# Kernel tuning notes

Measured on AMD Instinct MI355X. Metric: run time of the kernel, lower is better.

The kernel has to match this reference:

```python
import jax, jax.numpy as jnp
import numpy as np

B, DZ, M_, N_ = 2048, 256, 64, 64
GAMMA, EPS, MAXITERS = 1.0, 1e-6, 1000


def sinkhorn(Mcost):
    # entropic OT with uniform marginals r=1/m, c=1/n (ddn sinkhorn, non-logspace)
    b, h, w = Mcost.shape
    r = 1.0 / h
    c = 1.0 / w
    P = jnp.exp(-GAMMA * Mcost)
    P = P / jnp.sum(P, axis=(1, 2), keepdims=True)

    def cond_fn(state):
        P, it, err = state
        return jnp.logical_and(it < MAXITERS, err > EPS)

    def body_fn(state):
        P, it, _ = state
        alpha = jnp.sum(P, axis=2, keepdims=True)   # row sums (B,h,1)
        P = P * (r / alpha)                          # row normalize to r
        beta = jnp.sum(P, axis=1, keepdims=True)    # col sums (B,1,w)
        err = jnp.max(jnp.abs(beta - c))
        # torch loop breaks BEFORE col-normalizing when converged
        P = jnp.where(err <= EPS, P, P * (c / beta))
        return P, it + 1, err

    init_err = jnp.array(jnp.inf, dtype=Mcost.dtype)
    P, _, _ = jax.lax.while_loop(cond_fn, body_fn, (P, jnp.array(0, jnp.int32), init_err))
    return P


def setup_inputs() -> dict:
    key = jax.random.key(0)
    ks = jax.random.split(key, 7)
    H = M_ * N_
    z = jax.random.normal(ks[0], (B, DZ), dtype=jnp.float32)
    W1 = jax.random.normal(ks[1], (DZ, H), dtype=jnp.float32) * (1.0 / np.sqrt(DZ))
    b1 = jnp.zeros((H,), jnp.float32)
    W2 = jax.random.normal(ks[2], (H, H), dtype=jnp.float32) * (1.0 / np.sqrt(H))
    b2 = jnp.zeros((H,), jnp.float32)
    W3 = jax.random.normal(ks[3], (H, H), dtype=jnp.float32) * (1.0 / np.sqrt(H))
    b3 = jnp.zeros((H,), jnp.float32)
    return {"z": z, "W1": W1, "b1": b1, "W2": W2, "b2": b2, "W3": W3, "b3": b3}


def reference(z, W1, b1, W2, b2, W3, b3):
    x = jax.nn.relu(z @ W1 + b1)
    x = jax.nn.relu(x @ W2 + b2)
    x = x @ W3 + b3
    x = x.reshape(z.shape[0], M_, N_)  # (B, m, n) cost matrix
    return sinkhorn(x)
```

## Files before the change

### kernel.cpp

```cpp
#include <hip/hip_runtime.h>
#include <hip/hip_bf16.h>

typedef unsigned short ushort_t;
typedef __attribute__((ext_vector_type(8))) short bf16x8;
typedef __attribute__((ext_vector_type(4))) float f32x4;

#define MDIM 2048
#define NDIM 4096

__device__ __forceinline__ ushort_t to_bf16(float f) {
    __hip_bfloat16 h = __float2bfloat16(f);
    return *reinterpret_cast<ushort_t*>(&h);
}

__global__ void cast_bf16_kernel(const float* __restrict__ in, ushort_t* __restrict__ out, int n) {
    int i = blockIdx.x * blockDim.x + threadIdx.x;
    if (i < n) out[i] = to_bf16(in[i]);
}

__global__ void transpose_cast_kernel(const float* __restrict__ W, ushort_t* __restrict__ WT,
                                      int K, int N) {
    __shared__ float tile[32][33];
    const int tx = threadIdx.x, ty = threadIdx.y;
    const int n0 = blockIdx.x * 32, k0 = blockIdx.y * 32;
#pragma unroll
    for (int r = 0; r < 4; ++r)
        tile[ty + r * 8][tx] = W[(size_t)(k0 + ty + r * 8) * N + n0 + tx];
    __syncthreads();
    const int t = ty * 32 + tx;
    const int nl = t >> 3;
    const int kc = (t & 7) * 4;
    ushort4 o;
    o.x = to_bf16(tile[kc + 0][nl]);
    o.y = to_bf16(tile[kc + 1][nl]);
    o.z = to_bf16(tile[kc + 2][nl]);
    o.w = to_bf16(tile[kc + 3][nl]);
    *reinterpret_cast<ushort4*>(&WT[(size_t)(n0 + nl) * K + k0 + kc]) = o;
}


#define GLD(gp, lp) __builtin_amdgcn_global_load_lds(                      \
        (const __attribute__((address_space(1))) void*)(gp),               \
        (__attribute__((address_space(3))) void*)(lp), 16, 0, 0)

#define MFMA(d, a, b) d = __builtin_amdgcn_mfma_f32_16x16x32_bf16(a, b, d, 0, 0, 0)

template <typename OutT, bool RELU>
__global__ __launch_bounds__(512, 2) void gemm_p8(const ushort_t* __restrict__ A,
                                                  const ushort_t* __restrict__ BT,
                                                  const float* __restrict__ bias,
                                                  OutT* __restrict__ C, int Kdim) {
    __shared__ __align__(16) ushort_t As[3][128 * 64];
    __shared__ __align__(16) ushort_t Bs[3][256 * 64];

    const int t = threadIdx.x;
    const int l = t & 63;
    const int w = t >> 6;
    const int l16 = l & 15;
    const int quad = l >> 4;
    const int wr = w >> 2;
    const int wc = w & 3;
    const int m0 = blockIdx.y * 128;
    const int n0 = blockIdx.x * 256;

    f32x4 acc[4][4];
#pragma unroll
    for (int i = 0; i < 4; ++i)
#pragma unroll
        for (int j = 0; j < 4; ++j) acc[i][j] = (f32x4){0.f, 0.f, 0.f, 0.f};

    const int srow = w * 8 + (l >> 3);
    const int scol = ((l & 7) ^ (l >> 3)) * 8;
    const ushort_t* gA0 = A  + (size_t)(m0 + srow) * Kdim + scol;
    const ushort_t* gA1 = A  + (size_t)(m0 + 64 + srow) * Kdim + scol;
    const ushort_t* gB0 = BT + (size_t)(n0 + srow) * Kdim + scol;
    const ushort_t* gB1 = BT + (size_t)(n0 + 64 + srow) * Kdim + scol;
    const ushort_t* gB2 = BT + (size_t)(n0 + 128 + srow) * Kdim + scol;
    const ushort_t* gB3 = BT + (size_t)(n0 + 192 + srow) * Kdim + scol;
    const int ldsW = w * 8 * 64;

    const int swz = l16 & 7;
#define LDA_(buf, i, kk) (*(const bf16x8*)&As[buf][(wr * 64 + (i) * 16 + l16) * 64 + ((((kk) * 4 + quad) ^ swz) * 8)])
#define LDB_(buf, j, kk) (*(const bf16x8*)&Bs[buf][(wc * 64 + (j) * 16 + l16) * 64 + ((((kk) * 4 + quad) ^ swz) * 8)])

#define STAGE_TILE(buf, koff) do {                      \
        GLD(gA0 + (koff), &As[buf][ldsW]);              \
        GLD(gA1 + (koff), &As[buf][ldsW + 64 * 64]);    \
        GLD(gB0 + (koff), &Bs[buf][ldsW]);              \
        GLD(gB1 + (koff), &Bs[buf][ldsW + 64 * 64]);    \
        GLD(gB2 + (koff), &Bs[buf][ldsW + 128 * 64]);   \
        GLD(gB3 + (koff), &Bs[buf][ldsW + 192 * 64]);   \
    } while (0)

#define PHASE_BEGIN()                                       \
        __builtin_amdgcn_s_barrier();                       \
        asm volatile("s_waitcnt lgkmcnt(0)" ::: "memory");  \
        __builtin_amdgcn_s_setprio(1)
#define PHASE_END()                                         \
        __builtin_amdgcn_s_setprio(0);                      \
        __builtin_amdgcn_s_barrier()

#define MFMA16()                                                   \
        MFMA(acc[0][0], a0, b0); MFMA(acc[0][1], a0, b1);          \
        MFMA(acc[0][2], a0, b2); MFMA(acc[0][3], a0, b3);          \
        MFMA(acc[1][0], a1, b0); MFMA(acc[1][1], a1, b1);          \
        MFMA(acc[1][2], a1, b2); MFMA(acc[1][3], a1, b3);          \
        MFMA(acc[2][0], a2, b0); MFMA(acc[2][1], a2, b1);          \
        MFMA(acc[2][2], a2, b2); MFMA(acc[2][3], a2, b3);          \
        MFMA(acc[3][0], a3, b0); MFMA(acc[3][1], a3, b1);          \
        MFMA(acc[3][2], a3, b2); MFMA(acc[3][3], a3, b3)

    const int nt = Kdim >> 6;

    STAGE_TILE(0, 0);
    STAGE_TILE(1, 64);
    asm volatile("s_waitcnt vmcnt(6)" ::: "memory");
    __builtin_amdgcn_s_barrier();

    for (int tt = 0; tt < nt; ++tt) {
        const int buf = tt % 3;
        const int nb = (tt + 2) % 3;
        const int koff = (tt + 2) << 6;
        const bool more = (tt + 2) < nt;

        bf16x8 a0, a1, a2, a3, b0, b1, b2, b3;

        a0 = LDA_(buf, 0, 0); a1 = LDA_(buf, 1, 0);
        a2 = LDA_(buf, 2, 0); a3 = LDA_(buf, 3, 0);
        b0 = LDB_(buf, 0, 0); b1 = LDB_(buf, 1, 0);
        b2 = LDB_(buf, 2, 0); b3 = LDB_(buf, 3, 0);
        if (more) {
            GLD(gA0 + koff, &As[nb][ldsW]);
            GLD(gA1 + koff, &As[nb][ldsW + 64 * 64]);
            GLD(gB0 + koff, &Bs[nb][ldsW]);
        }
        PHASE_BEGIN();
        MFMA16();
        PHASE_END();

        a0 = LDA_(buf, 0, 1); a1 = LDA_(buf, 1, 1);
        a2 = LDA_(buf, 2, 1); a3 = LDA_(buf, 3, 1);
        b0 = LDB_(buf, 0, 1); b1 = LDB_(buf, 1, 1);
        b2 = LDB_(buf, 2, 1); b3 = LDB_(buf, 3, 1);
        if (more) {
            GLD(gB1 + koff, &Bs[nb][ldsW + 64 * 64]);
            GLD(gB2 + koff, &Bs[nb][ldsW + 128 * 64]);
            GLD(gB3 + koff, &Bs[nb][ldsW + 192 * 64]);
        }
        PHASE_BEGIN();
        MFMA16();
        __builtin_amdgcn_s_setprio(0);
        if (tt + 1 < nt) {
            if (more) asm volatile("s_waitcnt vmcnt(6)" ::: "memory");
            else      asm volatile("s_waitcnt vmcnt(0)" ::: "memory");
        }
        __builtin_amdgcn_s_barrier();
    }

#pragma unroll
    for (int i = 0; i < 4; ++i) {
#pragma unroll
        for (int r = 0; r < 4; ++r) {
            const int grow = m0 + wr * 64 + i * 16 + quad * 4 + r;
#pragma unroll
            for (int j = 0; j < 4; ++j) {
                const int gcol = n0 + wc * 64 + j * 16 + l16;
                float v = acc[i][j][r] + bias[gcol];
                if (RELU) v = fmaxf(v, 0.0f);
                if constexpr (sizeof(OutT) == 2) {
                    C[(size_t)grow * NDIM + gcol] = to_bf16(v);
                } else {
                    C[(size_t)grow * NDIM + gcol] = v;
                }
            }
        }
    }
}

__device__ __forceinline__ float rdl(float v, int l) {
    return __uint_as_float(__builtin_amdgcn_readlane(__float_as_uint(v), l));
}

__global__ __launch_bounds__(64) void sinkhorn_kernel(float* __restrict__ PM) {
    __shared__ __align__(16) float T[64 * 65];
    const int l = threadIdx.x;
    float* base = PM + (size_t)blockIdx.x * 4096;

    float Kcol[64];
    float Krow[64];
#pragma unroll
    for (int r = 0; r < 64; ++r)
        Kcol[r] = __expf(-base[r * 64 + l]);
#pragma unroll
    for (int r = 0; r < 64; ++r)
        T[r * 65 + l] = Kcol[r];
    __syncthreads();
#pragma unroll
    for (int c = 0; c < 64; ++c)
        Krow[c] = T[l * 65 + c];

    float a = 0.0f, b = 1.0f;
    for (int it = 0; it < 1000; ++it) {
        float t1 = 0.0f;
#pragma unroll
        for (int c = 0; c < 64; ++c)
            t1 = fmaf(Krow[c], rdl(b, c), t1);
        a = 0.015625f / t1;

        float t2 = 0.0f;
#pragma unroll
        for (int r = 0; r < 64; ++r)
            t2 = fmaf(Kcol[r], rdl(a, r), t2);
        const float err = fabsf(b * t2 - 0.015625f);
        if (__ballot(err > 1e-6f) == 0ull) break;
        b = 0.015625f / t2;
    }

#pragma unroll
    for (int r = 0; r < 64; ++r)
        base[r * 64 + l] = rdl(a, r) * Kcol[r] * b;
}

extern "C" void kernel_launch(void* const* d_in, const int* in_sizes, int n_in,
                              void* d_out, int out_size, void* d_ws, size_t ws_size,
                              hipStream_t stream) {
    const float* z  = (const float*)d_in[0];
    const float* W1 = (const float*)d_in[1];
    const float* b1 = (const float*)d_in[2];
    const float* W2 = (const float*)d_in[3];
    const float* b2 = (const float*)d_in[4];
    const float* W3 = (const float*)d_in[5];
    const float* b3 = (const float*)d_in[6];
    float* out = (float*)d_out;
    char* ws = (char*)d_ws;

    ushort_t* W2T = (ushort_t*)(ws + 0);
    ushort_t* W3T = (ushort_t*)(ws + (size_t)33554432);
    ushort_t* C1b = (ushort_t*)(ws + (size_t)67108864);
    ushort_t* C2b = (ushort_t*)(ws + (size_t)83886080);
    ushort_t* Zb  = (ushort_t*)(ws + (size_t)100663296);
    ushort_t* W1T = (ushort_t*)(ws + (size_t)101711872);

    cast_bf16_kernel<<<2048, 256, 0, stream>>>(z, Zb, MDIM * 256);
    transpose_cast_kernel<<<dim3(128, 8), dim3(32, 8), 0, stream>>>(W1, W1T, 256, 4096);
    transpose_cast_kernel<<<dim3(128, 128), dim3(32, 8), 0, stream>>>(W2, W2T, 4096, 4096);
    transpose_cast_kernel<<<dim3(128, 128), dim3(32, 8), 0, stream>>>(W3, W3T, 4096, 4096);

    gemm_p8<ushort_t, true><<<dim3(NDIM / 256, MDIM / 128), 512, 0, stream>>>(Zb, W1T, b1, C1b, 256);
    gemm_p8<ushort_t, true><<<dim3(NDIM / 256, MDIM / 128), 512, 0, stream>>>(C1b, W2T, b2, C2b, 4096);
    gemm_p8<float, false><<<dim3(NDIM / 256, MDIM / 128), 512, 0, stream>>>(C2b, W3T, b3, out, 4096);

    sinkhorn_kernel<<<2048, 64, 0, stream>>>(out);
}
```

Measured before the change: 360.1 us.

## Replace ping-pong phase barriers with single-phase LDS load then MFMA per tile

The K-loop no longer splits into two phases with barriers, setprio and lgkmcnt waits. It now loads all sixteen A/B fragments for both k-substeps up front, issues all six global-to-LDS stages at once, then runs the 32 MFMAs and hits one barrier per tile, which is skipped on the last iteration. The aim is to cut barrier and priority overhead and leave instruction scheduling to the compiler. In exchange it holds twice as many fragment registers and drops the explicit interleaving of warp groups between memory and math phases.

```diff
diff --git a/kernel.cpp b/kernel.cpp
--- a/kernel.cpp
+++ b/kernel.cpp
@@ -80,8 +80,8 @@
     const int ldsW = w * 8 * 64;
 
     const int swz = l16 & 7;
-#define LDA_(buf, i, kk) (*(const bf16x8*)&As[buf][(wr * 64 + (i) * 16 + l16) * 64 + ((((kk) * 4 + quad) ^ swz) * 8)])
-#define LDB_(buf, j, kk) (*(const bf16x8*)&Bs[buf][(wc * 64 + (j) * 16 + l16) * 64 + ((((kk) * 4 + quad) ^ swz) * 8)])
+#define LDA_(base, i, kk) (*(const bf16x8*)&(base)[(wr * 64 + (i) * 16 + l16) * 64 + ((((kk) * 4 + quad) ^ swz) * 8)])
+#define LDB_(base, j, kk) (*(const bf16x8*)&(base)[(wc * 64 + (j) * 16 + l16) * 64 + ((((kk) * 4 + quad) ^ swz) * 8)])
 
 #define STAGE_TILE(buf, koff) do {                      \
         GLD(gA0 + (koff), &As[buf][ldsW]);              \
@@ -92,15 +92,7 @@
         GLD(gB3 + (koff), &Bs[buf][ldsW + 192 * 64]);   \
     } while (0)
 
-#define PHASE_BEGIN()                                       \
-        __builtin_amdgcn_s_barrier();                       \
-        asm volatile("s_waitcnt lgkmcnt(0)" ::: "memory");  \
-        __builtin_amdgcn_s_setprio(1)
-#define PHASE_END()                                         \
-        __builtin_amdgcn_s_setprio(0);                      \
-        __builtin_amdgcn_s_barrier()
-
-#define MFMA16()                                                   \
+#define MFMA16(a0, a1, a2, a3, b0, b1, b2, b3)                     \
         MFMA(acc[0][0], a0, b0); MFMA(acc[0][1], a0, b1);          \
         MFMA(acc[0][2], a0, b2); MFMA(acc[0][3], a0, b3);          \
         MFMA(acc[1][0], a1, b0); MFMA(acc[1][1], a1, b1);          \
@@ -123,38 +115,24 @@
         const int koff = (tt + 2) << 6;
         const bool more = (tt + 2) < nt;
 
-        bf16x8 a0, a1, a2, a3, b0, b1, b2, b3;
-
-        a0 = LDA_(buf, 0, 0); a1 = LDA_(buf, 1, 0);
-        a2 = LDA_(buf, 2, 0); a3 = LDA_(buf, 3, 0);
-        b0 = LDB_(buf, 0, 0); b1 = LDB_(buf, 1, 0);
-        b2 = LDB_(buf, 2, 0); b3 = LDB_(buf, 3, 0);
-        if (more) {
-            GLD(gA0 + koff, &As[nb][ldsW]);
-            GLD(gA1 + koff, &As[nb][ldsW + 64 * 64]);
-            GLD(gB0 + koff, &Bs[nb][ldsW]);
-        }
-        PHASE_BEGIN();
-        MFMA16();
-        PHASE_END();
-
-        a0 = LDA_(buf, 0, 1); a1 = LDA_(buf, 1, 1);
-        a2 = LDA_(buf, 2, 1); a3 = LDA_(buf, 3, 1);
-        b0 = LDB_(buf, 0, 1); b1 = LDB_(buf, 1, 1);
-        b2 = LDB_(buf, 2, 1); b3 = LDB_(buf, 3, 1);
-        if (more) {
-            GLD(gB1 + koff, &Bs[nb][ldsW + 64 * 64]);
-            GLD(gB2 + koff, &Bs[nb][ldsW + 128 * 64]);
-            GLD(gB3 + koff, &Bs[nb][ldsW + 192 * 64]);
-        }
-        PHASE_BEGIN();
-        MFMA16();
-        __builtin_amdgcn_s_setprio(0);
+        const ushort_t* __restrict__ Ab = &As[buf][0];
+        const ushort_t* __restrict__ Bb = &Bs[buf][0];
+
+        bf16x8 a00 = LDA_(Ab, 0, 0), a01 = LDA_(Ab, 1, 0), a02 = LDA_(Ab, 2, 0), a03 = LDA_(Ab, 3, 0);
+        bf16x8 b00 = LDB_(Bb, 0, 0), b01 = LDB_(Bb, 1, 0), b02 = LDB_(Bb, 2, 0), b03 = LDB_(Bb, 3, 0);
+        bf16x8 a10 = LDA_(Ab, 0, 1), a11 = LDA_(Ab, 1, 1), a12 = LDA_(Ab, 2, 1), a13 = LDA_(Ab, 3, 1);
+        bf16x8 b10 = LDB_(Bb, 0, 1), b11 = LDB_(Bb, 1, 1), b12 = LDB_(Bb, 2, 1), b13 = LDB_(Bb, 3, 1);
+
+        if (more) STAGE_TILE(nb, koff);
+
+        MFMA16(a00, a01, a02, a03, b00, b01, b02, b03);
+        MFMA16(a10, a11, a12, a13, b10, b11, b12, b13);
+
         if (tt + 1 < nt) {
             if (more) asm volatile("s_waitcnt vmcnt(6)" ::: "memory");
             else      asm volatile("s_waitcnt vmcnt(0)" ::: "memory");
+            __builtin_amdgcn_s_barrier();
         }
-        __builtin_amdgcn_s_barrier();
     }
 
 #pragma unroll
```

New measurement: 333.0 us. 7.5% less time.
